# Kernel optimization log

Hardware: AMD Instinct MI355X
Metric: run time of the kernel (lower is better)

Reference implementation:

```python
import jax, jax.numpy as jnp
from jax import lax
import numpy as np

B, H, W = 1024, 28, 28
EPS = 1e-5


def _conv(x, w, b):
    # 3x3, stride 1, pad 1, NCHW/OIHW
    y = lax.conv_general_dilated(x, w, (1, 1), ((1, 1), (1, 1)),
                                 dimension_numbers=('NCHW', 'OIHW', 'NCHW'))
    return y + b[None, :, None, None]


def _bn(x, g, b, m, v):
    # inference-mode batchnorm (affine with running stats)
    s = (g * lax.rsqrt(v + EPS))[None, :, None, None]
    return (x - m[None, :, None, None]) * s + b[None, :, None, None]


def _deform_sample(x, off):
    # x: [B,C,H,W], off: [B,18,H,W] ordered (y,x) per 3x3 tap
    Bs, C, Hs, Ws = x.shape
    off = off.reshape(Bs, 9, 2, Hs, Ws)
    k = jnp.arange(3, dtype=x.dtype) - 1.0
    ky = jnp.repeat(k, 3)  # [9]
    kx = jnp.tile(k, 3)    # [9]
    py = jnp.arange(Hs, dtype=x.dtype)[None, None, :, None] + ky[None, :, None, None] + off[:, :, 0]
    px = jnp.arange(Ws, dtype=x.dtype)[None, None, None, :] + kx[None, :, None, None] + off[:, :, 1]
    y0 = jnp.floor(py)
    x0 = jnp.floor(px)
    y1 = y0 + 1.0
    x1 = x0 + 1.0
    wy1 = py - y0
    wy0 = 1.0 - wy1
    wx1 = px - x0
    wx0 = 1.0 - wx1
    flat = x.reshape(Bs, C, Hs * Ws)

    def gather(yy, xx):
        valid = (yy >= 0) & (yy <= Hs - 1) & (xx >= 0) & (xx <= Ws - 1)
        yc = jnp.clip(yy, 0, Hs - 1).astype(jnp.int32)
        xc = jnp.clip(xx, 0, Ws - 1).astype(jnp.int32)
        idx = (yc * Ws + xc).reshape(Bs, -1)  # [B, 9*H*W]
        g = jax.vmap(lambda f, i: f[:, i])(flat, idx)  # [B, C, 9*H*W]
        return g.reshape(Bs, C, 9, Hs, Ws) * valid[:, None].astype(x.dtype)

    s = (gather(y0, x0) * (wy0 * wx0)[:, None]
         + gather(y0, x1) * (wy0 * wx1)[:, None]
         + gather(y1, x0) * (wy1 * wx0)[:, None]
         + gather(y1, x1) * (wy1 * wx1)[:, None])
    return s  # [B, C, 9, H, W]


def setup_inputs() -> dict:
    key = jax.random.key(0)
    ks = jax.random.split(key, 16)

    def rn(k, shape, s=0.05):
        return jax.random.normal(k, shape, jnp.float32) * s

    inp = {
        'x': jax.random.normal(ks[0], (B, 1, H, W), jnp.float32),
        'w_off': rn(ks[1], (18, 1, 3, 3)),
        'b_off': jnp.zeros((18,), jnp.float32),
        'w_dcn': rn(ks[2], (32, 1, 3, 3), 0.3),
        'b_dcn': rn(ks[3], (32,)),
        'w2': rn(ks[4], (64, 32, 3, 3), 0.06),
        'b2': rn(ks[5], (64,)),
        'w3': rn(ks[6], (128, 64, 3, 3), 0.04),
        'b3': rn(ks[7], (128,)),
        'w4': rn(ks[8], (128, 128, 3, 3), 0.03),
        'b4': rn(ks[9], (128,)),
        'w_fc': rn(ks[10], (10, 128), 0.09),
        'b_fc': rn(ks[11], (10,)),
    }
    chans = {'bn1': 32, 'bn2': 64, 'bn3': 128, 'bn4': 128}
    for i, (n, c) in enumerate(chans.items()):
        kk = jax.random.split(ks[12 + i], 4)
        inp[n + '_g'] = 1.0 + rn(kk[0], (c,), 0.1)
        inp[n + '_b'] = rn(kk[1], (c,), 0.1)
        inp[n + '_m'] = rn(kk[2], (c,), 0.1)
        inp[n + '_v'] = jax.random.uniform(kk[3], (c,), jnp.float32, 0.5, 1.5)
    return inp


def reference(x, w_off, b_off, w_dcn, b_dcn,
              bn1_g, bn1_b, bn1_m, bn1_v,
              w2, b2, bn2_g, bn2_b, bn2_m, bn2_v,
              w3, b3, bn3_g, bn3_b, bn3_m, bn3_v,
              w4, b4, bn4_g, bn4_b, bn4_m, bn4_v,
              w_fc, b_fc):
    off = _conv(x, w_off, b_off)                      # [B,18,H,W]
    s = _deform_sample(x, off)                        # [B,1,9,H,W]
    h = jnp.einsum('bckhw,ock->bohw', s, w_dcn.reshape(32, 1, 9))
    h = h + b_dcn[None, :, None, None]
    h = _bn(h, bn1_g, bn1_b, bn1_m, bn1_v)
    h = _bn(jax.nn.relu(_conv(h, w2, b2)), bn2_g, bn2_b, bn2_m, bn2_v)
    h = _bn(jax.nn.relu(_conv(h, w3, b3)), bn3_g, bn3_b, bn3_m, bn3_v)
    h = _bn(jax.nn.relu(_conv(h, w4, b4)), bn4_g, bn4_b, bn4_m, bn4_v)
    pooled = h.mean(axis=(2, 3))                      # avg_pool k=28 == global mean
    logits = pooled @ w_fc.T + b_fc
    return jax.nn.log_softmax(logits, axis=1)
```

## Files before the change

kernel.cpp:

```cpp
#include <hip/hip_runtime.h>
#include <hip/hip_bf16.h>

typedef __bf16 bf16x8 __attribute__((ext_vector_type(8)));
typedef float  f32x4  __attribute__((ext_vector_type(4)));

#define BN_EPS 1e-5f

constexpr size_t ACT_PER_IMG = 57600 + 115200 + 230400;
constexpr size_t SZ_POOL = (size_t)1024 * 128 * 4;
constexpr size_t SZ_W2   = (size_t)9 * 64 * 32 * 2;
constexpr size_t SZ_W3   = (size_t)9 * 128 * 64 * 2;
constexpr size_t SZ_W4   = (size_t)9 * 128 * 128 * 2;
constexpr size_t SZ_BN   = 704 * 4;
constexpr size_t SZ_FIXED = SZ_POOL + SZ_W2 + SZ_W3 + SZ_W4 + SZ_BN;

__device__ __forceinline__ unsigned pack2(float a, float b) {
    __hip_bfloat162 h = __float22bfloat162_rn(make_float2(a, b));
    union { __hip_bfloat162 h2; unsigned u; } u;
    u.h2 = h;
    return u.u;
}

struct PrepArgs {
    const float *w2, *w3, *w4;
    const float *g1, *b1, *m1, *v1;
    const float *g2, *b2, *m2, *v2;
    const float *g3, *b3, *m3, *v3;
    const float *g4, *b4, *m4, *v4;
    __hip_bfloat16 *W2, *W3, *W4;
    float *bn;
};

__global__ __launch_bounds__(256) void prep_k(PrepArgs a) {
    int idx = blockIdx.x * 256 + threadIdx.x;
    if (idx < 18432) {
        int e = idx & 7, lane = (idx >> 3) & 63, r = idx >> 9;
        int nb = r & 3, t = r >> 2;
        int o = nb * 16 + (lane & 15);
        int i = (lane >> 4) * 8 + e;
        a.W2[idx] = __float2bfloat16(a.w2[(o * 32 + i) * 9 + t]);
        return;
    }
    idx -= 18432;
    if (idx < 73728) {
        int e = idx & 7, lane = (idx >> 3) & 63, r = idx >> 9;
        int nb = r & 7, s = r >> 3;
        int kc = s & 1, t = s >> 1;
        int o = nb * 16 + (lane & 15);
        int i = kc * 32 + (lane >> 4) * 8 + e;
        a.W3[idx] = __float2bfloat16(a.w3[(o * 64 + i) * 9 + t]);
        return;
    }
    idx -= 73728;
    if (idx < 147456) {
        int e = idx & 7, lane = (idx >> 3) & 63, r = idx >> 9;
        int nb = r & 7, s = r >> 3;
        int kc = s & 3, t = s >> 2;
        int o = nb * 16 + (lane & 15);
        int i = kc * 32 + (lane >> 4) * 8 + e;
        a.W4[idx] = __float2bfloat16(a.w4[(o * 128 + i) * 9 + t]);
        return;
    }
    idx -= 147456;
    if (idx < 352) {
        const float *g, *bb, *mm, *vv; int c, so, cn;
        if (idx < 32)       { g = a.g1; bb = a.b1; mm = a.m1; vv = a.v1; c = idx;       so = 0;   cn = 32;  }
        else if (idx < 96)  { g = a.g2; bb = a.b2; mm = a.m2; vv = a.v2; c = idx - 32;  so = 64;  cn = 64;  }
        else if (idx < 224) { g = a.g3; bb = a.b3; mm = a.m3; vv = a.v3; c = idx - 96;  so = 192; cn = 128; }
        else                { g = a.g4; bb = a.b4; mm = a.m4; vv = a.v4; c = idx - 224; so = 448; cn = 128; }
        float s = g[c] * rsqrtf(vv[c] + BN_EPS);
        a.bn[so + c] = s;
        a.bn[so + cn + c] = bb[c] - mm[c] * s;
    }
}

__global__ __launch_bounds__(256) void deform_k(
    const float* __restrict__ x, const float* __restrict__ w_off,
    const float* __restrict__ b_off, const float* __restrict__ w_dcn,
    const float* __restrict__ b_dcn, const float* __restrict__ bn,
    __hip_bfloat16* __restrict__ act1, __hip_bfloat16* __restrict__ act2,
    __hip_bfloat16* __restrict__ act3, float* __restrict__ pooled, int b0)
{
    const int lb = blockIdx.x;
    const int b  = b0 + lb;
    const int tid = threadIdx.x;
    __shared__ float xp[900];
    __shared__ float sw[564];
    float* swo = sw;
    float* sbo = sw + 162;
    float* swd = sw + 180;
    float* sbd = sw + 468;
    float* ss1 = sw + 500;
    float* ssh = sw + 532;

    for (int i = tid; i < 900; i += 256) {
        int y = i / 30, xc = i % 30;
        float v = 0.f;
        if (y >= 1 && y <= 28 && xc >= 1 && xc <= 28)
            v = x[(size_t)b * 784 + (y - 1) * 28 + (xc - 1)];
        xp[i] = v;
    }
    for (int i = tid; i < 564; i += 256) {
        float v;
        if (i < 162)      v = w_off[i];
        else if (i < 180) v = b_off[i - 162];
        else if (i < 468) v = w_dcn[i - 180];
        else if (i < 500) v = b_dcn[i - 468];
        else if (i < 532) v = bn[i - 500];
        else              v = bn[32 + (i - 532)];
        sw[i] = v;
    }
    if (tid < 128) pooled[b * 128 + tid] = 0.f;
    __syncthreads();

    for (int p = tid; p < 784; p += 256) {
        int y = p / 28, xx = p % 28;
        float off[18];
        #pragma unroll
        for (int o = 0; o < 18; o++) off[o] = sbo[o];
        #pragma unroll
        for (int ty = 0; ty < 3; ty++)
            #pragma unroll
            for (int tx = 0; tx < 3; tx++) {
                float xv = xp[(y + ty) * 30 + (xx + tx)];
                int tap = ty * 3 + tx;
                #pragma unroll
                for (int o = 0; o < 18; o++) off[o] = fmaf(xv, swo[o * 9 + tap], off[o]);
            }
        float s[9];
        #pragma unroll
        for (int j = 0; j < 9; j++) {
            float py = (float)y + (float)(j / 3 - 1) + off[2 * j];
            float px = (float)xx + (float)(j % 3 - 1) + off[2 * j + 1];
            float y0 = floorf(py), x0 = floorf(px);
            float wy1 = py - y0, wx1 = px - x0;
            float wy0 = 1.f - wy1, wx0 = 1.f - wx1;
            float acc = 0.f;
            #pragma unroll
            for (int cy = 0; cy < 2; cy++)
                #pragma unroll
                for (int cx = 0; cx < 2; cx++) {
                    float yy = y0 + (float)cy, xf = x0 + (float)cx;
                    bool valid = (yy >= 0.f) && (yy <= 27.f) && (xf >= 0.f) && (xf <= 27.f);
                    int yc = (int)fminf(fmaxf(yy, 0.f), 27.f);
                    int xc = (int)fminf(fmaxf(xf, 0.f), 27.f);
                    float g = valid ? xp[(yc + 1) * 30 + (xc + 1)] : 0.f;
                    float w = (cy ? wy1 : wy0) * (cx ? wx1 : wx0);
                    acc = fmaf(g, w, acc);
                }
            s[j] = acc;
        }
        size_t base = ((size_t)lb * 900 + (size_t)(y + 1) * 30 + (xx + 1)) * 32;
        #pragma unroll
        for (int c0 = 0; c0 < 32; c0 += 8) {
            float h[8];
            #pragma unroll
            for (int ci = 0; ci < 8; ci++) {
                int c = c0 + ci;
                float hv = sbd[c];
                #pragma unroll
                for (int j = 0; j < 9; j++) hv = fmaf(s[j], swd[c * 9 + j], hv);
                h[ci] = hv * ss1[c] + ssh[c];
            }
            uint4 q;
            q.x = pack2(h[0], h[1]); q.y = pack2(h[2], h[3]);
            q.z = pack2(h[4], h[5]); q.w = pack2(h[6], h[7]);
            *reinterpret_cast<uint4*>(&act1[base + c0]) = q;
        }
    }

    for (int i = tid; i < 116; i += 256) {
        int py, px;
        if (i < 30)      { py = 0;          px = i; }
        else if (i < 60) { py = 29;         px = i - 30; }
        else if (i < 88) { py = i - 60 + 1; px = 0; }
        else             { py = i - 88 + 1; px = 29; }
        size_t pix = (size_t)lb * 900 + (size_t)py * 30 + px;
        uint4 z = {0, 0, 0, 0};
        uint4* p1 = reinterpret_cast<uint4*>(&act1[pix * 32]);
        #pragma unroll
        for (int k = 0; k < 4; k++) p1[k] = z;
        uint4* p2 = reinterpret_cast<uint4*>(&act2[pix * 64]);
        #pragma unroll
        for (int k = 0; k < 8; k++) p2[k] = z;
        uint4* p3 = reinterpret_cast<uint4*>(&act3[pix * 128]);
        #pragma unroll
        for (int k = 0; k < 16; k++) p3[k] = z;
    }
}

template<int CIN>
__device__ __forceinline__ int swz(int ofs) {
    if constexpr (CIN == 128) return (ofs >> 4) & 0x70;
    else if constexpr (CIN == 64) return (ofs >> 3) & 0x70;
    else return (ofs >> 2) & 0x30;
}

template<int COUT, int NFW>
__device__ __forceinline__ void loadWf(const __hip_bfloat16* __restrict__ Wt,
                                       int s, int nq, int lane, bf16x8 (&bf)[NFW]) {
    constexpr int NB = COUT / 16;
    #pragma unroll
    for (int nf = 0; nf < NFW; ++nf)
        bf[nf] = *reinterpret_cast<const bf16x8*>(
            Wt + (((size_t)s * NB + nq * NFW + nf) * 64 + lane) * 8);
}

template<int CIN, int MFW>
__device__ __forceinline__ void loadAf(const __hip_bfloat16* tile,
                                       int s, const int (&pr)[4], const int (&pc)[4],
                                       int kg, bf16x8 (&af)[MFW]) {
    constexpr int KC = CIN / 32;
    int t = s / KC, kc = (s % KC) * 32;
    int ty = t / 3, tx = t % 3;
    #pragma unroll
    for (int mf = 0; mf < MFW; ++mf) {
        int pix = (pr[mf] + ty) * 30 + (pc[mf] + tx);
        int ba = (pix * CIN + kc + kg * 8) * 2;
        ba ^= swz<CIN>(ba);
        af[mf] = *reinterpret_cast<const bf16x8*>(
            reinterpret_cast<const char*>(tile) + ba);
    }
}

template<int MFW, int NFW>
__device__ __forceinline__ void mstep(const bf16x8 (&af)[MFW], const bf16x8 (&wf)[NFW],
                                      f32x4 (&acc)[MFW][NFW]) {
    #pragma unroll
    for (int mf = 0; mf < MFW; ++mf)
        #pragma unroll
        for (int nf = 0; nf < NFW; ++nf)
            acc[mf][nf] = __builtin_amdgcn_mfma_f32_16x16x32_bf16(
                af[mf], wf[nf], acc[mf][nf], 0, 0, 0);
}

template<int CIN, int COUT, bool POOL, int MFW>
__device__ __forceinline__ void conv_body(
    const __hip_bfloat16* tile,
    const __hip_bfloat16* __restrict__ Wt,
    const float* __restrict__ bconv, const float* __restrict__ bnS,
    const float* __restrict__ bnB, __hip_bfloat16* __restrict__ aout,
    float* __restrict__ pooled, int lb, int gb, int rg, int lane, int mhalf, int nq)
{
    constexpr int KC  = CIN / 32;
    constexpr int NS  = 9 * KC;
    constexpr int NFW = COUT / 64;
    const int l15 = lane & 15, kg = lane >> 4;
    const int nbase = nq * (NFW * 16) + l15;

    int pr[4], pc[4];
    #pragma unroll
    for (int mf = 0; mf < MFW; ++mf) {
        int m = (mhalf * 4 + mf) * 16 + l15;
        pr[mf] = m / 28;
        pc[mf] = m % 28;
    }

    f32x4 acc[MFW][NFW] = {};
    bf16x8 w0[NFW], w1[NFW], a0[MFW];

    loadWf<COUT, NFW>(Wt, 0, nq, lane, w0);
    #pragma unroll
    for (int s = 0; s < NS; s += 2) {
        loadAf<CIN, MFW>(tile, s, pr, pc, kg, a0);
        if (s + 1 < NS) loadWf<COUT, NFW>(Wt, s + 1, nq, lane, w1);
        mstep<MFW, NFW>(a0, w0, acc);
        if (s + 1 < NS) {
            loadAf<CIN, MFW>(tile, s + 1, pr, pc, kg, a0);
            if (s + 2 < NS) loadWf<COUT, NFW>(Wt, s + 2, nq, lane, w0);
            mstep<MFW, NFW>(a0, w1, acc);
        }
    }

    if constexpr (!POOL) {
        #pragma unroll
        for (int mf = 0; mf < MFW; ++mf) {
            #pragma unroll
            for (int nf = 0; nf < NFW; ++nf) {
                int n = nbase + nf * 16;
                float bc = bconv[n], sc = bnS[n], sh = bnB[n];
                #pragma unroll
                for (int r = 0; r < 4; r++) {
                    int m = (mhalf * 4 + mf) * 16 + kg * 4 + r;
                    float y = acc[mf][nf][r] + bc;
                    y = fmaxf(y, 0.f);
                    y = y * sc + sh;
                    int oy = m / 28, ox = m % 28;
                    aout[((size_t)lb * 900 + (size_t)(rg * 4 + oy + 1) * 30 + (ox + 1)) * COUT + n]
                        = __float2bfloat16(y);
                }
            }
        }
    } else {
        #pragma unroll
        for (int nf = 0; nf < NFW; ++nf) {
            int n = nbase + nf * 16;
            float bc = bconv[n], sc = bnS[n], sh = bnB[n];
            float ps = 0.f;
            #pragma unroll
            for (int mf = 0; mf < MFW; ++mf)
                #pragma unroll
                for (int r = 0; r < 4; r++) {
                    float y = acc[mf][nf][r] + bc;
                    y = fmaxf(y, 0.f);
                    ps += y * sc + sh;
                }
            ps += __shfl_xor(ps, 16, 64);
            ps += __shfl_xor(ps, 32, 64);
            if (lane < 16) atomicAdd(&pooled[gb * COUT + n], ps);
        }
    }
}

template<int CIN, int COUT, bool POOL>
__global__ __launch_bounds__(512, 4) void conv_k(
    const __hip_bfloat16* __restrict__ ain,
    const __hip_bfloat16* __restrict__ Wt,
    const float* __restrict__ bconv,
    const float* __restrict__ bnS,
    const float* __restrict__ bnB,
    __hip_bfloat16* __restrict__ aout,
    float* __restrict__ pooled, int b0, int nimg)
{
    __shared__ __align__(16) __hip_bfloat16 tile[180 * CIN];
    const int tid = threadIdx.x;
    const int lane = tid & 63;
    const int wv = tid >> 6;
    const int mhalf = wv >> 2;
    const int nq = wv & 3;

    int rg, lb;
    {
        int flat = blockIdx.x + 7 * blockIdx.y;
        if ((nimg & 7) == 0) {
            int xcd = flat & 7, idx = flat >> 3;
            lb = xcd * (nimg >> 3) + idx / 7;
            rg = idx % 7;
        } else {
            rg = blockIdx.x; lb = blockIdx.y;
        }
    }

    const char* src = reinterpret_cast<const char*>(
        ain + ((size_t)lb * 900 + (size_t)rg * 120) * CIN);
    constexpr int TB = 180 * CIN * 2;
    for (int ofs = tid * 16; ofs < TB; ofs += 8192) {
        uint4 v = *reinterpret_cast<const uint4*>(src + ofs);
        *reinterpret_cast<uint4*>(reinterpret_cast<char*>(tile) + (ofs ^ swz<CIN>(ofs))) = v;
    }
    __syncthreads();

    if (mhalf == 0)
        conv_body<CIN, COUT, POOL, 4>(tile, Wt, bconv, bnS, bnB, aout, pooled,
                                      lb, b0 + lb, rg, lane, mhalf, nq);
    else
        conv_body<CIN, COUT, POOL, 3>(tile, Wt, bconv, bnS, bnB, aout, pooled,
                                      lb, b0 + lb, rg, lane, mhalf, nq);
}

__global__ __launch_bounds__(256) void head_k(
    const float* __restrict__ pooled, const float* __restrict__ wfc,
    const float* __restrict__ bfc, float* __restrict__ out)
{
    int b = blockIdx.x * 4 + (threadIdx.x >> 6);
    int lane = threadIdx.x & 63;
    float m0 = pooled[b * 128 + lane] * (1.f / 784.f);
    float m1 = pooled[b * 128 + 64 + lane] * (1.f / 784.f);
    float lg[10];
    #pragma unroll
    for (int k = 0; k < 10; k++) {
        float p = m0 * wfc[k * 128 + lane] + m1 * wfc[k * 128 + 64 + lane];
        #pragma unroll
        for (int s2 = 32; s2 >= 1; s2 >>= 1) p += __shfl_xor(p, s2, 64);
        lg[k] = p + bfc[k];
    }
    float mx = lg[0];
    #pragma unroll
    for (int k = 1; k < 10; k++) mx = fmaxf(mx, lg[k]);
    float se = 0.f;
    #pragma unroll
    for (int k = 0; k < 10; k++) se += expf(lg[k] - mx);
    float lse = mx + logf(se);
    #pragma unroll
    for (int k = 0; k < 10; k++)
        if (lane == k) out[b * 10 + k] = lg[k] - lse;
}

extern "C" void kernel_launch(void* const* d_in, const int* in_sizes, int n_in,
                              void* d_out, int out_size, void* d_ws, size_t ws_size,
                              hipStream_t stream) {
    (void)in_sizes; (void)n_in; (void)out_size;
    const float* x     = (const float*)d_in[0];
    const float* w_off = (const float*)d_in[1];
    const float* b_off = (const float*)d_in[2];
    const float* w_dcn = (const float*)d_in[3];
    const float* b_dcn = (const float*)d_in[4];
    const float* w2    = (const float*)d_in[5];
    const float* b2    = (const float*)d_in[6];
    const float* w3    = (const float*)d_in[7];
    const float* b3    = (const float*)d_in[8];
    const float* w4    = (const float*)d_in[9];
    const float* b4    = (const float*)d_in[10];
    const float* w_fc  = (const float*)d_in[11];
    const float* b_fc  = (const float*)d_in[12];

    int CH = 256;
    while (CH > 1 && (size_t)CH * ACT_PER_IMG + SZ_FIXED > ws_size) CH >>= 1;
    const int NCHUNK = 1024 / CH;

    char* ws = (char*)d_ws;
    const size_t szA1 = (size_t)CH * 57600;
    const size_t szA2 = (size_t)CH * 115200;
    const size_t szA3 = (size_t)CH * 230400;
    __hip_bfloat16* act1 = (__hip_bfloat16*)(ws);
    __hip_bfloat16* act2 = (__hip_bfloat16*)(ws + szA1);
    __hip_bfloat16* act3 = (__hip_bfloat16*)(ws + szA1 + szA2);
    float* pooled        = (float*)(ws + szA1 + szA2 + szA3);
    __hip_bfloat16* W2   = (__hip_bfloat16*)(ws + szA1 + szA2 + szA3 + SZ_POOL);
    __hip_bfloat16* W3   = (__hip_bfloat16*)((char*)W2 + SZ_W2);
    __hip_bfloat16* W4   = (__hip_bfloat16*)((char*)W3 + SZ_W3);
    float* bn            = (float*)((char*)W4 + SZ_W4);

    PrepArgs pa;
    pa.w2 = w2; pa.w3 = w3; pa.w4 = w4;
    pa.g1 = (const float*)d_in[13]; pa.b1 = (const float*)d_in[14];
    pa.m1 = (const float*)d_in[15]; pa.v1 = (const float*)d_in[16];
    pa.g2 = (const float*)d_in[17]; pa.b2 = (const float*)d_in[18];
    pa.m2 = (const float*)d_in[19]; pa.v2 = (const float*)d_in[20];
    pa.g3 = (const float*)d_in[21]; pa.b3 = (const float*)d_in[22];
    pa.m3 = (const float*)d_in[23]; pa.v3 = (const float*)d_in[24];
    pa.g4 = (const float*)d_in[25]; pa.b4 = (const float*)d_in[26];
    pa.m4 = (const float*)d_in[27]; pa.v4 = (const float*)d_in[28];
    pa.W2 = W2; pa.W3 = W3; pa.W4 = W4; pa.bn = bn;

    prep_k<<<938, 256, 0, stream>>>(pa);
    for (int c = 0; c < NCHUNK; ++c) {
        int b0 = c * CH;
        deform_k<<<CH, 256, 0, stream>>>(x, w_off, b_off, w_dcn, b_dcn, bn,
                                         act1, act2, act3, pooled, b0);
        conv_k<32, 64, false><<<dim3(7, CH), 512, 0, stream>>>(
            act1, W2, b2, bn + 64, bn + 128, act2, nullptr, b0, CH);
        conv_k<64, 128, false><<<dim3(7, CH), 512, 0, stream>>>(
            act2, W3, b3, bn + 192, bn + 320, act3, nullptr, b0, CH);
        conv_k<128, 128, true><<<dim3(7, CH), 512, 0, stream>>>(
            act3, W4, b4, bn + 448, bn + 576, nullptr, pooled, b0, CH);
    }
    head_k<<<256, 256, 0, stream>>>(pooled, w_fc, b_fc, (float*)d_out);
}
```

Measured before the change: 671.6 us.

## Use 2-wave conv blocks with larger per-wave tiles and double-buffered fragments

```diff
diff --git a/kernel.cpp b/kernel.cpp
--- a/kernel.cpp
+++ b/kernel.cpp
@@ -206,15 +206,15 @@
             Wt + (((size_t)s * NB + nq * NFW + nf) * 64 + lane) * 8);
 }
 
-template<int CIN, int MFW>
+template<int CIN>
 __device__ __forceinline__ void loadAf(const __hip_bfloat16* tile,
-                                       int s, const int (&pr)[4], const int (&pc)[4],
-                                       int kg, bf16x8 (&af)[MFW]) {
+                                       int s, const int (&pr)[7], const int (&pc)[7],
+                                       int kg, bf16x8 (&af)[7]) {
     constexpr int KC = CIN / 32;
     int t = s / KC, kc = (s % KC) * 32;
     int ty = t / 3, tx = t % 3;
     #pragma unroll
-    for (int mf = 0; mf < MFW; ++mf) {
+    for (int mf = 0; mf < 7; ++mf) {
         int pix = (pr[mf] + ty) * 30 + (pc[mf] + tx);
         int ba = (pix * CIN + kc + kg * 8) * 2;
         ba ^= swz<CIN>(ba);
@@ -223,65 +223,75 @@
     }
 }
 
-template<int MFW, int NFW>
-__device__ __forceinline__ void mstep(const bf16x8 (&af)[MFW], const bf16x8 (&wf)[NFW],
-                                      f32x4 (&acc)[MFW][NFW]) {
-    #pragma unroll
-    for (int mf = 0; mf < MFW; ++mf)
+template<int NFW>
+__device__ __forceinline__ void mstep7(const bf16x8 (&af)[7], const bf16x8 (&wf)[NFW],
+                                       f32x4 (&acc)[7][NFW]) {
+    #pragma unroll
+    for (int mf = 0; mf < 7; ++mf)
         #pragma unroll
         for (int nf = 0; nf < NFW; ++nf)
             acc[mf][nf] = __builtin_amdgcn_mfma_f32_16x16x32_bf16(
                 af[mf], wf[nf], acc[mf][nf], 0, 0, 0);
 }
 
-template<int CIN, int COUT, bool POOL, int MFW>
+template<int CIN, int COUT, bool POOL>
 __device__ __forceinline__ void conv_body(
     const __hip_bfloat16* tile,
     const __hip_bfloat16* __restrict__ Wt,
     const float* __restrict__ bconv, const float* __restrict__ bnS,
     const float* __restrict__ bnB, __hip_bfloat16* __restrict__ aout,
-    float* __restrict__ pooled, int lb, int gb, int rg, int lane, int mhalf, int nq)
+    float* __restrict__ pooled, int lb, int gb, int rg, int lane, int nq)
 {
     constexpr int KC  = CIN / 32;
     constexpr int NS  = 9 * KC;
-    constexpr int NFW = COUT / 64;
+    constexpr int NFW = COUT / 32;
     const int l15 = lane & 15, kg = lane >> 4;
     const int nbase = nq * (NFW * 16) + l15;
 
-    int pr[4], pc[4];
-    #pragma unroll
-    for (int mf = 0; mf < MFW; ++mf) {
-        int m = (mhalf * 4 + mf) * 16 + l15;
+    int pr[7], pc[7];
+    #pragma unroll
+    for (int mf = 0; mf < 7; ++mf) {
+        int m = mf * 16 + l15;
         pr[mf] = m / 28;
         pc[mf] = m % 28;
     }
 
-    f32x4 acc[MFW][NFW] = {};
-    bf16x8 w0[NFW], w1[NFW], a0[MFW];
-
-    loadWf<COUT, NFW>(Wt, 0, nq, lane, w0);
+    f32x4 acc[7][NFW] = {};
+    bf16x8 wA[NFW], wB[NFW], aA[7], aB[7];
+
+    loadWf<COUT, NFW>(Wt, 0, nq, lane, wA);
+    loadAf<CIN>(tile, 0, pr, pc, kg, aA);
+    loadWf<COUT, NFW>(Wt, 1, nq, lane, wB);
+    loadAf<CIN>(tile, 1, pr, pc, kg, aB);
+
     #pragma unroll
     for (int s = 0; s < NS; s += 2) {
-        loadAf<CIN, MFW>(tile, s, pr, pc, kg, a0);
-        if (s + 1 < NS) loadWf<COUT, NFW>(Wt, s + 1, nq, lane, w1);
-        mstep<MFW, NFW>(a0, w0, acc);
+        __builtin_amdgcn_sched_barrier(0);
+        mstep7<NFW>(aA, wA, acc);
+        if (s + 2 < NS) {
+            loadWf<COUT, NFW>(Wt, s + 2, nq, lane, wA);
+            loadAf<CIN>(tile, s + 2, pr, pc, kg, aA);
+        }
+        __builtin_amdgcn_sched_barrier(0);
         if (s + 1 < NS) {
-            loadAf<CIN, MFW>(tile, s + 1, pr, pc, kg, a0);
-            if (s + 2 < NS) loadWf<COUT, NFW>(Wt, s + 2, nq, lane, w0);
-            mstep<MFW, NFW>(a0, w1, acc);
+            mstep7<NFW>(aB, wB, acc);
+            if (s + 3 < NS) {
+                loadWf<COUT, NFW>(Wt, s + 3, nq, lane, wB);
+                loadAf<CIN>(tile, s + 3, pr, pc, kg, aB);
+            }
         }
     }
 
     if constexpr (!POOL) {
         #pragma unroll
-        for (int mf = 0; mf < MFW; ++mf) {
+        for (int mf = 0; mf < 7; ++mf) {
             #pragma unroll
             for (int nf = 0; nf < NFW; ++nf) {
                 int n = nbase + nf * 16;
                 float bc = bconv[n], sc = bnS[n], sh = bnB[n];
                 #pragma unroll
                 for (int r = 0; r < 4; r++) {
-                    int m = (mhalf * 4 + mf) * 16 + kg * 4 + r;
+                    int m = mf * 16 + kg * 4 + r;
                     float y = acc[mf][nf][r] + bc;
                     y = fmaxf(y, 0.f);
                     y = y * sc + sh;
@@ -298,7 +308,7 @@
             float bc = bconv[n], sc = bnS[n], sh = bnB[n];
             float ps = 0.f;
             #pragma unroll
-            for (int mf = 0; mf < MFW; ++mf)
+            for (int mf = 0; mf < 7; ++mf)
                 #pragma unroll
                 for (int r = 0; r < 4; r++) {
                     float y = acc[mf][nf][r] + bc;
@@ -313,7 +323,7 @@
 }
 
 template<int CIN, int COUT, bool POOL>
-__global__ __launch_bounds__(512, 4) void conv_k(
+__global__ __launch_bounds__(128, 2) void conv_k(
     const __hip_bfloat16* __restrict__ ain,
     const __hip_bfloat16* __restrict__ Wt,
     const float* __restrict__ bconv,
@@ -325,9 +335,7 @@
     __shared__ __align__(16) __hip_bfloat16 tile[180 * CIN];
     const int tid = threadIdx.x;
     const int lane = tid & 63;
-    const int wv = tid >> 6;
-    const int mhalf = wv >> 2;
-    const int nq = wv & 3;
+    const int nq = tid >> 6;
 
     int rg, lb;
     {
@@ -344,18 +352,14 @@
     const char* src = reinterpret_cast<const char*>(
         ain + ((size_t)lb * 900 + (size_t)rg * 120) * CIN);
     constexpr int TB = 180 * CIN * 2;
-    for (int ofs = tid * 16; ofs < TB; ofs += 8192) {
+    for (int ofs = tid * 16; ofs < TB; ofs += 2048) {
         uint4 v = *reinterpret_cast<const uint4*>(src + ofs);
         *reinterpret_cast<uint4*>(reinterpret_cast<char*>(tile) + (ofs ^ swz<CIN>(ofs))) = v;
     }
     __syncthreads();
 
-    if (mhalf == 0)
-        conv_body<CIN, COUT, POOL, 4>(tile, Wt, bconv, bnS, bnB, aout, pooled,
-                                      lb, b0 + lb, rg, lane, mhalf, nq);
-    else
-        conv_body<CIN, COUT, POOL, 3>(tile, Wt, bconv, bnS, bnB, aout, pooled,
-                                      lb, b0 + lb, rg, lane, mhalf, nq);
+    conv_body<CIN, COUT, POOL>(tile, Wt, bconv, bnS, bnB, aout, pooled,
+                               lb, b0 + lb, rg, lane, nq);
 }
 
 __global__ __launch_bounds__(256) void head_k(
@@ -438,11 +442,11 @@
         int b0 = c * CH;
         deform_k<<<CH, 256, 0, stream>>>(x, w_off, b_off, w_dcn, b_dcn, bn,
                                          act1, act2, act3, pooled, b0);
-        conv_k<32, 64, false><<<dim3(7, CH), 512, 0, stream>>>(
+        conv_k<32, 64, false><<<dim3(7, CH), 128, 0, stream>>>(
             act1, W2, b2, bn + 64, bn + 128, act2, nullptr, b0, CH);
-        conv_k<64, 128, false><<<dim3(7, CH), 512, 0, stream>>>(
+        conv_k<64, 128, false><<<dim3(7, CH), 128, 0, stream>>>(
             act2, W3, b3, bn + 192, bn + 320, act3, nullptr, b0, CH);
-        conv_k<128, 128, true><<<dim3(7, CH), 512, 0, stream>>>(
+        conv_k<128, 128, true><<<dim3(7, CH), 128, 0, stream>>>(
             act3, W4, b4, bn + 448, bn + 576, nullptr, pooled, b0, CH);
     }
     head_k<<<256, 256, 0, stream>>>(pooled, w_fc, b_fc, (float*)d_out);
```

Result: faster. 648.0 us (-3.5%).
